# Optimization experiments

Hardware: AMD Instinct MI355X
Metric: run time of the kernel (lower is better)

Reference implementation:

```python
import jax, jax.numpy as jnp
import numpy as np

D_MODEL, D_K, D_V, BLOCK = 1024, 128, 128, 2048
B, T = 8, 2048

def setup_inputs() -> dict:
    key = jax.random.key(0)
    kx, kq, kk, kv = jax.random.split(key, 4)
    # nn.Linear weights are [out_features, in_features]
    s = 1.0 / np.sqrt(D_MODEL)
    return {
        "x": jax.random.normal(kx, (B, T, D_MODEL), dtype=jnp.float32),
        "W_q": jax.random.uniform(kq, (D_K, D_MODEL), jnp.float32, -s, s),
        "W_k": jax.random.uniform(kk, (D_K, D_MODEL), jnp.float32, -s, s),
        "W_v": jax.random.uniform(kv, (D_V, D_MODEL), jnp.float32, -s, s),
    }

def reference(x, W_q, W_k, W_v) -> jnp.ndarray:
    Tlen = x.shape[1]
    Q = jnp.einsum('btc,kc->btk', x, W_q)   # [B,T,d_k]
    K = jnp.einsum('btc,kc->btk', x, W_k)   # [B,T,d_k]
    V = jnp.einsum('btc,vc->btv', x, W_v)   # [B,T,d_v]
    scores = jnp.einsum('bqk,bsk->bqs', Q, K) / jnp.sqrt(jnp.float32(D_K))
    causal = jnp.tril(jnp.ones((Tlen, Tlen), dtype=bool))[None, :, :]
    scores = jnp.where(causal, scores, jnp.finfo(scores.dtype).min)
    attn = jax.nn.softmax(scores, axis=-1)
    return jnp.einsum('bqs,bsv->bqv', attn, V)  # [B,T,d_v]
```

## Files before the change

### kernel.cpp

```cpp
#include <hip/hip_runtime.h>
#include <hip/hip_fp16.h>

typedef _Float16 half8  __attribute__((ext_vector_type(8)));
typedef _Float16 half4v __attribute__((ext_vector_type(4)));
typedef float    f32x4  __attribute__((ext_vector_type(4)));

#define MFMA_F16 __builtin_amdgcn_mfma_f32_16x16x32_f16

#define BAR_VM4() asm volatile("s_waitcnt vmcnt(4)\n\ts_barrier" ::: "memory")
#define BAR_VM0() asm volatile("s_waitcnt vmcnt(0)\n\ts_barrier" ::: "memory")

__device__ __forceinline__ unsigned pack_f16(float a, float b) {
    union { __fp16 h __attribute__((ext_vector_type(2))); unsigned u; } cv;
    cv.h = __builtin_amdgcn_cvt_pkrtz(a, b);
    return cv.u;
}

__device__ __forceinline__ void gload16(const void* g, void* l) {
    __builtin_amdgcn_global_load_lds((const __attribute__((address_space(1))) void*)g,
                                     (__attribute__((address_space(3))) void*)l, 16, 0, 0);
}

__global__ __launch_bounds__(256) void wconv_k(const float* __restrict__ wq,
                                               const float* __restrict__ wk,
                                               const float* __restrict__ wv,
                                               _Float16* __restrict__ wh) {
    int i = (blockIdx.x * 256 + threadIdx.x) * 8;
    const float* src; int off;
    if (i < 131072)      { src = wq; off = i; }
    else if (i < 262144) { src = wk; off = i - 131072; }
    else                 { src = wv; off = i - 262144; }
    float4 a = *(const float4*)(src + off);
    float4 b = *(const float4*)(src + off + 4);
    half8 h;
    h[0]=(_Float16)a.x; h[1]=(_Float16)a.y; h[2]=(_Float16)a.z; h[3]=(_Float16)a.w;
    h[4]=(_Float16)b.x; h[5]=(_Float16)b.y; h[6]=(_Float16)b.z; h[7]=(_Float16)b.w;
    *(half8*)(wh + i) = h;
}

__global__ __launch_bounds__(256, 3) void qkv_k(const float* __restrict__ x,
                                                const _Float16* __restrict__ wh,
                                                _Float16* __restrict__ qh,
                                                _Float16* __restrict__ kh,
                                                _Float16* __restrict__ vth) {
    __shared__ float    xs[3][64 * 32];
    __shared__ _Float16 wsb[3][128 * 32];
    const int tid = threadIdx.x;
    const int w = tid >> 6, l = tid & 63;
    const int fr = l & 15, fq = l >> 4;
    const int bid = blockIdx.x;
    const int xcd = bid & 7;
    const int slot = bid >> 3;
    const int rb = (slot / 3) * 8 + xcd;
    const int cb = slot % 3;
    const int row0 = rb * 64;
    const int c0 = cb * 128 + w * 32;
    const int xk = (fr & 7) << 4;

    int xrow[2], xcol[2];
#pragma unroll
    for (int i = 0; i < 2; ++i) {
        int ob = i * 4096 + tid * 16;
        xrow[i] = ob >> 7;
        xcol[i] = ((ob & 127) ^ ((xrow[i] & 7) << 4)) >> 2;
    }
    int wrow_[2], wcol_[2];
#pragma unroll
    for (int i = 0; i < 2; ++i) {
        int ob = i * 4096 + tid * 16;
        wrow_[i] = ob >> 6;
        wcol_[i] = ((ob & 63) ^ ((wrow_[i] & 3) << 4)) >> 1;
    }

    f32x4 acc[4][2] = {};

#define STAGE(kt, bb) do {                                                                \
    _Pragma("unroll")                                                                     \
    for (int i = 0; i < 2; ++i)                                                           \
        gload16(x + (row0 + xrow[i]) * 1024 + (kt) * 32 + xcol[i],                        \
                (char*)(&xs[bb][0]) + i * 4096 + tid * 16);                               \
    _Pragma("unroll")                                                                     \
    for (int i = 0; i < 2; ++i)                                                           \
        gload16(wh + (cb * 128 + wrow_[i]) * 1024 + (kt) * 32 + wcol_[i],                 \
                (char*)(&wsb[bb][0]) + i * 4096 + tid * 16);                              \
    } while (0)

    STAGE(0, 0);
    STAGE(1, 1);

    int rd = 0, stg = 2;
    for (int kt = 0; kt < 32; ++kt) {
        if (kt < 31) BAR_VM4();
        else         BAR_VM0();
        if (kt + 2 < 32) STAGE(kt + 2, stg);

        const char* xb = (const char*)(&xs[rd][0]);
        const char* wb = (const char*)(&wsb[rd][0]);
        half8 af[4];
#pragma unroll
        for (int mf = 0; mf < 4; ++mf) {
            const char* rp = xb + (mf * 16 + fr) * 128;
            float4 a0 = *(const float4*)(rp + ((fq * 32) ^ xk));
            float4 a1 = *(const float4*)(rp + ((fq * 32 + 16) ^ xk));
            union { unsigned u[4]; half8 h; } cv;
            cv.u[0] = pack_f16(a0.x, a0.y);
            cv.u[1] = pack_f16(a0.z, a0.w);
            cv.u[2] = pack_f16(a1.x, a1.y);
            cv.u[3] = pack_f16(a1.z, a1.w);
            af[mf] = cv.h;
        }
        half8 bf[2];
#pragma unroll
        for (int nf = 0; nf < 2; ++nf) {
            int wr = w * 32 + nf * 16 + fr;
            bf[nf] = *(const half8*)(wb + wr * 64 + ((fq * 16) ^ ((wr & 3) << 4)));
        }
        __builtin_amdgcn_s_setprio(1);
#pragma unroll
        for (int mf = 0; mf < 4; ++mf)
#pragma unroll
            for (int nf = 0; nf < 2; ++nf)
                acc[mf][nf] = MFMA_F16(af[mf], bf[nf], acc[mf][nf], 0, 0, 0);
        __builtin_amdgcn_s_setprio(0);

        stg = rd;
        rd = (rd == 2) ? 0 : rd + 1;
    }
#undef STAGE

#pragma unroll
    for (int nf = 0; nf < 2; ++nf) {
        int n0 = c0 + nf * 16 + fr;
#pragma unroll
        for (int mf = 0; mf < 4; ++mf) {
            int mb = row0 + mf * 16 + fq * 4;
            if (cb == 0) {
#pragma unroll
                for (int r = 0; r < 4; ++r) qh[(mb + r) * 128 + n0] = (_Float16)acc[mf][nf][r];
            } else if (cb == 1) {
#pragma unroll
                for (int r = 0; r < 4; ++r) kh[(mb + r) * 128 + (n0 - 128)] = (_Float16)acc[mf][nf][r];
            } else {
                half4v pv;
#pragma unroll
                for (int r = 0; r < 4; ++r) pv[r] = (_Float16)acc[mf][nf][r];
                int t = mb & 2047;
                int tl = t & 63;
                int tp = (t & ~63) | (tl & 35) | ((tl & 12) << 1) | ((tl & 16) >> 2);
                *(half4v*)(&vth[((mb >> 11) * 128 + (n0 - 256)) * 2048 + tp]) = pv;
            }
        }
    }
}

#define BAR_VMA() asm volatile("s_waitcnt vmcnt(0)\n\ts_barrier" ::: "memory")
__global__ __launch_bounds__(512, 4) void attn_k(const _Float16* __restrict__ qh,
                                                 const _Float16* __restrict__ kh,
                                                 const _Float16* __restrict__ vth,
                                                 _Float16* __restrict__ part,
                                                 float* __restrict__ stats,
                                                 float* __restrict__ out) {
    __shared__ _Float16 ks[2][32 * 128];
    __shared__ _Float16 vs[2][128 * 32];

    int bid = blockIdx.x;
    int b = bid & 7;
    int u = bid >> 3;
    int qt, c;
    {
        int idx = u;
        qt = 0;
        for (;;) { int nc = (qt >> 1) + 1; if (idx < nc) break; idx -= nc; ++qt; }
        c = idx;
    }
    int j0 = c * 8;
    int jmax = 4 * qt + 4;
    int j1 = j0 + 8 < jmax ? j0 + 8 : jmax;

    int tid = threadIdx.x, w = tid >> 6, l = tid & 63;
    int fr = l & 15, fq = l >> 4;
    int xw = (fr & 7) << 4;
    int xv = (fr & 3) << 4;

    const int kr  = tid >> 4;
    const int kc  = (tid & 15) ^ (kr & 7);
    const int vdd = tid >> 2;
    const int vc  = (tid & 3) ^ (vdd & 3);

    half8 qf[4];
    const _Float16* qp = qh + ((b * 2048 + qt * 128 + w * 16 + fr) << 7);
#pragma unroll
    for (int cc = 0; cc < 4; ++cc) qf[cc] = *(const half8*)(qp + cc * 32 + fq * 8);

#define GLOAD_TILE(j, bb) do {                                                            \
    gload16(kh + (((b << 11) + ((j) << 5) + kr) << 7) + kc * 8, &ks[bb][0] + w * 512);    \
    gload16(vth + (((b << 7) + vdd) << 11) + ((j) << 5) + vc * 8, &vs[bb][0] + w * 512);  \
    } while (0)

    f32x4 acc[8] = {};
    float mrow = -1e30f, lrow = 0.0f;

    GLOAD_TILE(j0, 0);
    BAR_VMA();
    if (j0 + 1 < j1) GLOAD_TILE(j0 + 1, 1);

    int cur = 0;
    for (int j = j0; j < j1; ++j) {
        const char* ksb = (const char*)(ks[cur]);
        const char* vsb = (const char*)(vs[cur]);

        f32x4 s[2] = {};
        __builtin_amdgcn_s_setprio(1);
#pragma unroll
        for (int n = 0; n < 2; ++n) {
            const char* krow = ksb + (n * 16 + fr) * 256;
#pragma unroll
            for (int cc = 0; cc < 4; ++cc) {
                half8 kf = *(const half8*)(krow + ((cc * 64 + fq * 16) ^ xw));
                s[n] = MFMA_F16(kf, qf[cc], s[n], 0, 0, 0);
            }
        }
        __builtin_amdgcn_s_setprio(0);
        const float sc = 0.088388347648318447f;
        if (j >= 4 * qt) {
            int koff = (j - 4 * qt) << 5;
            int qrow = w * 16 + fr;
#pragma unroll
            for (int n = 0; n < 2; ++n)
#pragma unroll
                for (int r = 0; r < 4; ++r) {
                    int kcol = koff + n * 16 + fq * 4 + r;
                    float v = s[n][r] * sc;
                    s[n][r] = (kcol > qrow) ? -1e30f : v;
                }
        } else {
#pragma unroll
            for (int n = 0; n < 2; ++n)
#pragma unroll
                for (int r = 0; r < 4; ++r) s[n][r] *= sc;
        }

        float pmax = s[0][0];
#pragma unroll
        for (int n = 0; n < 2; ++n)
#pragma unroll
            for (int r = 0; r < 4; ++r) pmax = fmaxf(pmax, s[n][r]);
        float al = 1.0f;
        if (!__all(pmax - mrow <= 8.0f)) {
            float mx = pmax;
            mx = fmaxf(mx, __shfl_xor(mx, 16));
            mx = fmaxf(mx, __shfl_xor(mx, 32));
            float nm = fmaxf(mrow, mx);
            al = __expf(mrow - nm);
            mrow = nm;
#pragma unroll
            for (int dt = 0; dt < 8; ++dt)
#pragma unroll
                for (int r = 0; r < 4; ++r) acc[dt][r] *= al;
        }
        float rs = 0.f;
#pragma unroll
        for (int n = 0; n < 2; ++n)
#pragma unroll
            for (int r = 0; r < 4; ++r) {
                float p = __expf(s[n][r] - mrow);
                s[n][r] = p;
                rs += p;
            }
        rs += __shfl_xor(rs, 16);
        rs += __shfl_xor(rs, 32);
        lrow = lrow * al + rs;

        union { unsigned u[4]; half8 h; } pb;
        pb.u[0] = pack_f16(s[0][0], s[0][1]);
        pb.u[1] = pack_f16(s[0][2], s[0][3]);
        pb.u[2] = pack_f16(s[1][0], s[1][1]);
        pb.u[3] = pack_f16(s[1][2], s[1][3]);

        __builtin_amdgcn_s_setprio(1);
#pragma unroll
        for (int dt = 0; dt < 8; ++dt) {
            const char* vrow = vsb + (dt * 16 + fr) * 64;
            half8 vf = *(const half8*)(vrow + ((fq * 16) ^ xv));
            acc[dt] = MFMA_F16(vf, pb.h, acc[dt], 0, 0, 0);
        }
        __builtin_amdgcn_s_setprio(0);

        BAR_VMA();
        if (j + 2 < j1) GLOAD_TILE(j + 2, cur);
        cur ^= 1;
    }

    float inv = 1.0f / lrow;

    if (qt < 2) {
        float* op = out + ((b * 2048 + qt * 128 + w * 16 + fr) << 7) + fq * 4;
#pragma unroll
        for (int dt = 0; dt < 8; ++dt) {
            float4 o;
            o.x = acc[dt][0] * inv; o.y = acc[dt][1] * inv;
            o.z = acc[dt][2] * inv; o.w = acc[dt][3] * inv;
            *(float4*)(op + dt * 16) = o;
        }
    } else {
        _Float16* op = part + bid * 16384 + w * 2048 + l * 4;
#pragma unroll
        for (int dt = 0; dt < 8; ++dt) {
            half4v h;
#pragma unroll
            for (int r = 0; r < 4; ++r) h[r] = (_Float16)(acc[dt][r] * inv);
            *(half4v*)(op + dt * 256) = h;
        }
        if (l < 16) {
            int ridx = bid * 128 + w * 16 + l;
            float2 st; st.x = mrow; st.y = lrow;
            *(float2*)(&stats[ridx * 2]) = st;
        }
    }
#undef GLOAD_TILE
}

__global__ __launch_bounds__(256) void comb_k(const _Float16* __restrict__ part,
                                              const float* __restrict__ stats,
                                              float* __restrict__ out) {
    int bid = blockIdx.x;
    int b = bid & 7;
    int rest = bid >> 3;
    int qt = 2 + (rest >> 2);
    int rh = rest & 3;
    int h = qt >> 1;
    int nc = h + 1;
    int u0 = qt + h * (h - 1) + (qt & 1) * h;
    int t = threadIdx.x;
    int row = rh * 32 + (t >> 3), g = t & 7;
    int w = row >> 4, q16 = row & 15;

    float mstar = -1e30f, mv[8], lv[8];
#pragma unroll
    for (int cc = 0; cc < 8; ++cc) {
        if (cc < nc) {
            int sidx = (((u0 + cc) << 3) + b) * 128 + row;
            mv[cc] = stats[sidx * 2];
            lv[cc] = stats[sidx * 2 + 1];
            mstar = fmaxf(mstar, mv[cc]);
        }
    }
    float den = 0.f, wc[8];
#pragma unroll
    for (int cc = 0; cc < 8; ++cc) {
        if (cc < nc) { wc[cc] = __expf(mv[cc] - mstar) * lv[cc]; den += wc[cc]; }
        else wc[cc] = 0.f;
    }
    float a[16] = {};
#pragma unroll
    for (int cc = 0; cc < 8; ++cc) {
        if (cc < nc) {
            const _Float16* pp = part + ((((u0 + cc) << 3) + b) * 16384) + w * 2048 + g * 256;
            float wcc = wc[cc];
#pragma unroll
            for (int fq = 0; fq < 4; ++fq) {
                half4v hh = *(const half4v*)(pp + (fq * 16 + q16) * 4);
#pragma unroll
                for (int r = 0; r < 4; ++r)
                    a[fq * 4 + r] += wcc * (float)hh[r];
            }
        }
    }
    float id = 1.0f / den;
    float* op = out + (b * 2048 + qt * 128 + row) * 128 + g * 16;
#pragma unroll
    for (int uu = 0; uu < 4; ++uu) {
        float4 o;
        o.x = a[uu * 4]     * id;
        o.y = a[uu * 4 + 1] * id;
        o.z = a[uu * 4 + 2] * id;
        o.w = a[uu * 4 + 3] * id;
        *(float4*)(op + uu * 4) = o;
    }
}

extern "C" void kernel_launch(void* const* d_in, const int* in_sizes, int n_in,
                              void* d_out, int out_size, void* d_ws, size_t ws_size,
                              hipStream_t stream) {
    const float* x  = (const float*)d_in[0];
    const float* wq = (const float*)d_in[1];
    const float* wk = (const float*)d_in[2];
    const float* wv = (const float*)d_in[3];

    char* ws = (char*)d_ws;
    _Float16* wh   = (_Float16*)(ws);
    _Float16* qhp  = (_Float16*)(ws + (1u  << 20));
    _Float16* khp  = (_Float16*)(ws + (5u  << 20));
    _Float16* vtp  = (_Float16*)(ws + (9u  << 20));
    _Float16* part = (_Float16*)(ws + (13u << 20));
    float*    stat = (float*)   (ws + (32u << 20));

    wconv_k<<<192, 256, 0, stream>>>(wq, wk, wv, wh);
    qkv_k<<<768, 256, 0, stream>>>(x, wh, qhp, khp, vtp);
    attn_k<<<576, 512, 0, stream>>>(qhp, khp, vtp, part, stat, (float*)d_out);
    comb_k<<<448, 256, 0, stream>>>(part, stat, (float*)d_out);
}
```

Measured before the change: 72.21 us.

## Retile QKV projection into single-wave 32x64 blocks without barriers

Recasts the QKV projection kernel from 256-thread blocks with 64x128 tiles into 64-thread single-wavefront blocks computing 32x64 tiles, launching four times as many blocks. With one wave per block, the s_barrier in the triple-buffered pipeline is dropped and only vmcnt waits remain. The prefetch of stage kt+2 moves after the LDS fragment reads. This removes cross-wave synchronization but lowers reuse: x rows are now reloaded by six column groups instead of three, and each weight slice is shared by fewer rows.

```diff
diff --git a/kernel.cpp b/kernel.cpp
--- a/kernel.cpp
+++ b/kernel.cpp
@@ -6,9 +6,6 @@
 typedef float    f32x4  __attribute__((ext_vector_type(4)));
 
 #define MFMA_F16 __builtin_amdgcn_mfma_f32_16x16x32_f16
-
-#define BAR_VM4() asm volatile("s_waitcnt vmcnt(4)\n\ts_barrier" ::: "memory")
-#define BAR_VM0() asm volatile("s_waitcnt vmcnt(0)\n\ts_barrier" ::: "memory")
 
 __device__ __forceinline__ unsigned pack_f16(float a, float b) {
     union { __fp16 h __attribute__((ext_vector_type(2))); unsigned u; } cv;
@@ -38,67 +35,66 @@
     *(half8*)(wh + i) = h;
 }
 
-__global__ __launch_bounds__(256, 3) void qkv_k(const float* __restrict__ x,
-                                                const _Float16* __restrict__ wh,
-                                                _Float16* __restrict__ qh,
-                                                _Float16* __restrict__ kh,
-                                                _Float16* __restrict__ vth) {
-    __shared__ float    xs[3][64 * 32];
-    __shared__ _Float16 wsb[3][128 * 32];
+__global__ __launch_bounds__(64, 4) void qkv_k(const float* __restrict__ x,
+                                               const _Float16* __restrict__ wh,
+                                               _Float16* __restrict__ qh,
+                                               _Float16* __restrict__ kh,
+                                               _Float16* __restrict__ vth) {
+    __shared__ float    xs[3][32 * 32];
+    __shared__ _Float16 wsb[3][64 * 32];
     const int tid = threadIdx.x;
-    const int w = tid >> 6, l = tid & 63;
-    const int fr = l & 15, fq = l >> 4;
+    const int fr = tid & 15, fq = (tid >> 4) & 3;
     const int bid = blockIdx.x;
     const int xcd = bid & 7;
     const int slot = bid >> 3;
-    const int rb = (slot / 3) * 8 + xcd;
-    const int cb = slot % 3;
-    const int row0 = rb * 64;
-    const int c0 = cb * 128 + w * 32;
+    const int rg = (slot / 6) * 8 + xcd;
+    const int cg = slot % 6;
+    const int row0 = rg * 32;
+    const int c0 = cg * 64;
     const int xk = (fr & 7) << 4;
 
-    int xrow[2], xcol[2];
-#pragma unroll
-    for (int i = 0; i < 2; ++i) {
-        int ob = i * 4096 + tid * 16;
+    int xrow[4], xcol[4];
+#pragma unroll
+    for (int i = 0; i < 4; ++i) {
+        int ob = i * 1024 + tid * 16;
         xrow[i] = ob >> 7;
         xcol[i] = ((ob & 127) ^ ((xrow[i] & 7) << 4)) >> 2;
     }
-    int wrow_[2], wcol_[2];
-#pragma unroll
-    for (int i = 0; i < 2; ++i) {
-        int ob = i * 4096 + tid * 16;
+    int wrow_[4], wcol_[4];
+#pragma unroll
+    for (int i = 0; i < 4; ++i) {
+        int ob = i * 1024 + tid * 16;
         wrow_[i] = ob >> 6;
         wcol_[i] = ((ob & 63) ^ ((wrow_[i] & 3) << 4)) >> 1;
     }
 
-    f32x4 acc[4][2] = {};
+    f32x4 acc[2][4] = {};
 
 #define STAGE(kt, bb) do {                                                                \
     _Pragma("unroll")                                                                     \
-    for (int i = 0; i < 2; ++i)                                                           \
+    for (int i = 0; i < 4; ++i)                                                           \
         gload16(x + (row0 + xrow[i]) * 1024 + (kt) * 32 + xcol[i],                        \
-                (char*)(&xs[bb][0]) + i * 4096 + tid * 16);                               \
+                (char*)(&xs[bb][0]) + i * 1024 + tid * 16);                               \
     _Pragma("unroll")                                                                     \
-    for (int i = 0; i < 2; ++i)                                                           \
-        gload16(wh + (cb * 128 + wrow_[i]) * 1024 + (kt) * 32 + wcol_[i],                 \
-                (char*)(&wsb[bb][0]) + i * 4096 + tid * 16);                              \
+    for (int i = 0; i < 4; ++i)                                                           \
+        gload16(wh + (c0 + wrow_[i]) * 1024 + (kt) * 32 + wcol_[i],                       \
+                (char*)(&wsb[bb][0]) + i * 1024 + tid * 16);                              \
     } while (0)
 
     STAGE(0, 0);
     STAGE(1, 1);
 
-    int rd = 0, stg = 2;
     for (int kt = 0; kt < 32; ++kt) {
-        if (kt < 31) BAR_VM4();
-        else         BAR_VM0();
-        if (kt + 2 < 32) STAGE(kt + 2, stg);
-
+        if (kt < 31) asm volatile("s_waitcnt vmcnt(8)" ::: "memory");
+        else         asm volatile("s_waitcnt vmcnt(0)" ::: "memory");
+
+        const int rd = kt % 3;
         const char* xb = (const char*)(&xs[rd][0]);
         const char* wb = (const char*)(&wsb[rd][0]);
-        half8 af[4];
-#pragma unroll
-        for (int mf = 0; mf < 4; ++mf) {
+
+        half8 af[2];
+#pragma unroll
+        for (int mf = 0; mf < 2; ++mf) {
             const char* rp = xb + (mf * 16 + fr) * 128;
             float4 a0 = *(const float4*)(rp + ((fq * 32) ^ xk));
             float4 a1 = *(const float4*)(rp + ((fq * 32 + 16) ^ xk));
@@ -109,35 +105,35 @@
             cv.u[3] = pack_f16(a1.z, a1.w);
             af[mf] = cv.h;
         }
-        half8 bf[2];
-#pragma unroll
-        for (int nf = 0; nf < 2; ++nf) {
-            int wr = w * 32 + nf * 16 + fr;
+        half8 bf[4];
+#pragma unroll
+        for (int nf = 0; nf < 4; ++nf) {
+            int wr = nf * 16 + fr;
             bf[nf] = *(const half8*)(wb + wr * 64 + ((fq * 16) ^ ((wr & 3) << 4)));
         }
+
+        if (kt + 2 < 32) STAGE(kt + 2, (kt + 2) % 3);
+
         __builtin_amdgcn_s_setprio(1);
 #pragma unroll
-        for (int mf = 0; mf < 4; ++mf)
-#pragma unroll
-            for (int nf = 0; nf < 2; ++nf)
+        for (int mf = 0; mf < 2; ++mf)
+#pragma unroll
+            for (int nf = 0; nf < 4; ++nf)
                 acc[mf][nf] = MFMA_F16(af[mf], bf[nf], acc[mf][nf], 0, 0, 0);
         __builtin_amdgcn_s_setprio(0);
-
-        stg = rd;
-        rd = (rd == 2) ? 0 : rd + 1;
     }
 #undef STAGE
 
 #pragma unroll
-    for (int nf = 0; nf < 2; ++nf) {
+    for (int nf = 0; nf < 4; ++nf) {
         int n0 = c0 + nf * 16 + fr;
 #pragma unroll
-        for (int mf = 0; mf < 4; ++mf) {
+        for (int mf = 0; mf < 2; ++mf) {
             int mb = row0 + mf * 16 + fq * 4;
-            if (cb == 0) {
+            if (cg < 2) {
 #pragma unroll
                 for (int r = 0; r < 4; ++r) qh[(mb + r) * 128 + n0] = (_Float16)acc[mf][nf][r];
-            } else if (cb == 1) {
+            } else if (cg < 4) {
 #pragma unroll
                 for (int r = 0; r < 4; ++r) kh[(mb + r) * 128 + (n0 - 128)] = (_Float16)acc[mf][nf][r];
             } else {
@@ -396,7 +392,7 @@
     float*    stat = (float*)   (ws + (32u << 20));
 
     wconv_k<<<192, 256, 0, stream>>>(wq, wk, wv, wh);
-    qkv_k<<<768, 256, 0, stream>>>(x, wh, qhp, khp, vtp);
+    qkv_k<<<3072, 64, 0, stream>>>(x, wh, qhp, khp, vtp);
     attn_k<<<576, 512, 0, stream>>>(qhp, khp, vtp, part, stat, (float*)d_out);
     comb_k<<<448, 256, 0, stream>>>(part, stat, (float*)d_out);
 }
```

Result: slower. 86.04 us (+19.1%).
